# Kernel optimization log

Hardware: AMD Instinct MI355X
Metric: run time of the kernel (lower is better)

The kernel has to match this reference:

```python
import jax, jax.numpy as jnp
import numpy as np
import math

D_MODEL = 32    # channels; expand=1 => d_inner == d_model
D_STATE = 8
D_CONV = 4
DT_RANK = math.ceil(D_MODEL / 16)  # 2


def _layernorm(x, g, b, eps=1e-5):
    m = jnp.mean(x, axis=-1, keepdims=True)
    v = jnp.var(x, axis=-1, keepdims=True)
    return (x - m) * jax.lax.rsqrt(v + eps) * g + b


def _causal_dwconv(x, w, b):
    # x: [B, D, L], w: [D, 1, K] depthwise causal conv (pad K-1 on the left)
    y = jax.lax.conv_general_dilated(
        x, w, window_strides=(1,), padding=[(D_CONV - 1, 0)],
        dimension_numbers=('NCH', 'OIH', 'NCH'),
        feature_group_count=x.shape[1])
    return y + b[None, :, None]


def _ssm_branch(xb, z, conv_w, conv_b, xproj_w, dtproj_w, dtproj_b, A_log, Dp):
    # One mamba_inner (no out_proj) branch. xb, z: [B, D, L]
    Bsz, Dd, L = xb.shape
    u = jax.nn.silu(_causal_dwconv(xb, conv_w, conv_b))              # [B,D,L]
    x_dbl = jnp.einsum('bdl,rd->blr', u, xproj_w)                    # [B,L,R+2N]
    dt = x_dbl[..., :DT_RANK]                                        # [B,L,R]
    Bm = x_dbl[..., DT_RANK:DT_RANK + D_STATE]                       # [B,L,N]
    Cm = x_dbl[..., DT_RANK + D_STATE:]                              # [B,L,N]
    delta = jax.nn.softplus(jnp.einsum('blr,dr->bld', dt, dtproj_w) + dtproj_b)  # [B,L,D]
    A = -jnp.exp(A_log)                                              # [D,N]

    def step(h, inp):
        d_l, u_l, B_l, C_l = inp   # [B,D], [B,D], [B,N], [B,N]
        dA = jnp.exp(d_l[..., None] * A)                             # [B,D,N]
        h = dA * h + (d_l * u_l)[..., None] * B_l[:, None, :]
        y = jnp.einsum('bdn,bn->bd', h, C_l)
        return h, y

    h0 = jnp.zeros((Bsz, Dd, D_STATE), dtype=xb.dtype)
    _, ys = jax.lax.scan(step, h0,
                         (delta.transpose(1, 0, 2), u.transpose(2, 0, 1),
                          Bm.transpose(1, 0, 2), Cm.transpose(1, 0, 2)))
    y = ys.transpose(1, 2, 0)                                        # [B,D,L]
    y = y + Dp[None, :, None] * u
    return y * jax.nn.silu(z)


def _forward(x, w1, b1, ln_g, ln_b, in_proj_w,
             conv_w_f, conv_b_f, xproj_w_f, dtproj_w_f, dtproj_b_f, A_log_f, D_f,
             conv_w_b, conv_b_b, xproj_w_b, dtproj_w_b, dtproj_b_b, A_log_b, D_b,
             norm_g, norm_b, out_proj_w, w2, b2):
    s = jnp.max(x, axis=(2, 3))                                      # AdaptiveMaxPool2d((1,1)) -> [B,L]
    h = s[..., None] * w1[None, None, :, 0] + b1                     # Linear(1, d_model) -> [B,L,D]
    h = _layernorm(h, ln_g, ln_b)
    # Mamba, bimamba v2
    xz = jnp.einsum('bld,ed->bel', h, in_proj_w)                     # [B,2D,L]
    x_f, z_f = jnp.split(xz, 2, axis=1)
    out_f = _ssm_branch(x_f, z_f, conv_w_f, conv_b_f, xproj_w_f,
                        dtproj_w_f, dtproj_b_f, A_log_f, D_f)
    xz_r = jnp.flip(xz, axis=-1)
    x_b, z_b = jnp.split(xz_r, 2, axis=1)
    out_b = _ssm_branch(x_b, z_b, conv_w_b, conv_b_b, xproj_w_b,
                        dtproj_w_b, dtproj_b_b, A_log_b, D_b)
    y = (out_f + jnp.flip(out_b, axis=-1)).transpose(0, 2, 1)        # [B,L,D]
    y = _layernorm(y, norm_g, norm_b) / 2.0                          # use_norm + if_devide_out
    y = jnp.einsum('bld,od->blo', y, out_proj_w)                     # out_proj -> [B,L,D]
    o = jnp.einsum('bld,od->blo', y, w2) + b2                        # Linear(d_model, 1) -> [B,L,1]
    return jax.nn.sigmoid(o)[..., None]                              # [B,L,1,1]


def setup_inputs() -> dict:
    key = jax.random.key(0)
    ks = jax.random.split(key, 16)
    B, Cin, H, W = 16, 128, 256, 256
    D, N, R = D_MODEL, D_STATE, DT_RANK

    def nrm(k, shp, s=0.2):
        return jax.random.normal(k, shp, dtype=jnp.float32) * s

    A_log_init = jnp.log(jnp.arange(1, N + 1, dtype=jnp.float32))[None, :] * jnp.ones((D, 1), jnp.float32)
    return dict(
        x=jax.random.normal(ks[0], (B, Cin, H, W), dtype=jnp.float32),
        w1=nrm(ks[1], (D, 1), 0.5), b1=nrm(ks[2], (D,), 0.1),
        ln_g=jnp.ones((D,), jnp.float32), ln_b=jnp.zeros((D,), jnp.float32),
        in_proj_w=nrm(ks[3], (2 * D, D)),
        conv_w_f=nrm(ks[4], (D, 1, D_CONV)), conv_b_f=nrm(ks[5], (D,), 0.1),
        xproj_w_f=nrm(ks[6], (R + 2 * N, D)),
        dtproj_w_f=nrm(ks[7], (D, R)), dtproj_b_f=nrm(ks[8], (D,), 0.1),
        A_log_f=A_log_init, D_f=jnp.ones((D,), jnp.float32),
        conv_w_b=nrm(ks[9], (D, 1, D_CONV)), conv_b_b=nrm(ks[10], (D,), 0.1),
        xproj_w_b=nrm(ks[11], (R + 2 * N, D)),
        dtproj_w_b=nrm(ks[12], (D, R)), dtproj_b_b=nrm(ks[13], (D,), 0.1),
        A_log_b=A_log_init, D_b=jnp.ones((D,), jnp.float32),
        norm_g=jnp.ones((D,), jnp.float32), norm_b=jnp.zeros((D,), jnp.float32),
        out_proj_w=nrm(ks[14], (D, D)),
        w2=nrm(ks[15], (1, D), 0.5), b2=jnp.zeros((1,), jnp.float32),
    )


def reference(x, w1, b1, ln_g, ln_b, in_proj_w,
              conv_w_f, conv_b_f, xproj_w_f, dtproj_w_f, dtproj_b_f, A_log_f, D_f,
              conv_w_b, conv_b_b, xproj_w_b, dtproj_w_b, dtproj_b_b, A_log_b, D_b,
              norm_g, norm_b, out_proj_w, w2, b2):
    return _forward(x, w1, b1, ln_g, ln_b, in_proj_w,
                    conv_w_f, conv_b_f, xproj_w_f, dtproj_w_f, dtproj_b_f, A_log_f, D_f,
                    conv_w_b, conv_b_b, xproj_w_b, dtproj_w_b, dtproj_b_b, A_log_b, D_b,
                    norm_g, norm_b, out_proj_w, w2, b2)
```

## Files before the change

### kernel.cpp

```cpp
#include <hip/hip_runtime.h>
#include <hip/hip_bf16.h>
#include <math.h>

#define B_SZ 16
#define L_SEQ 128
#define D_M 32
#define HW 65536
#define NROWS (B_SZ * 128)
#define NCHUNK 2

typedef float vfloat4 __attribute__((ext_vector_type(4)));

__device__ float g_part[NROWS * NCHUNK];
__device__ float g_y[2][B_SZ * D_M * L_SEQ];
__device__ int   g_done[B_SZ];

__device__ __forceinline__ float silu_acc(float x) {
    return x / (1.f + __expf(-x));
}
__device__ __forceinline__ float softplusf(float x) {
    return (x > 20.f) ? x : log1pf(__expf(x));
}

__device__ __forceinline__ float row_max(int row) {
    const int r2 = row * NCHUNK;
    return fmaxf(g_part[r2], g_part[r2 + 1]);
}

__device__ __forceinline__ void compute_h(int row, const float* __restrict__ w1,
                                          const float* __restrict__ b1,
                                          const float* __restrict__ lng,
                                          const float* __restrict__ lnb,
                                          float h[D_M]) {
    const float s = row_max(row);
    float mean = 0.f;
#pragma unroll
    for (int d = 0; d < D_M; d++) { h[d] = s * w1[d] + b1[d]; mean += h[d]; }
    mean *= (1.f / D_M);
    float var = 0.f;
#pragma unroll
    for (int d = 0; d < D_M; d++) { float t = h[d] - mean; var += t * t; }
    var *= (1.f / D_M);
    const float rs = rsqrtf(var + 1e-5f);
#pragma unroll
    for (int d = 0; d < D_M; d++) h[d] = (h[d] - mean) * rs * lng[d] + lnb[d];
}

__global__ __launch_bounds__(256) void kmax(const float* __restrict__ x) {
    const int blk = blockIdx.x;
    const vfloat4* __restrict__ p =
        reinterpret_cast<const vfloat4*>(x) + (size_t)blk * 8192;
    const int t = threadIdx.x;
    float m0 = -INFINITY, m1 = -INFINITY, m2 = -INFINITY, m3 = -INFINITY;
#pragma unroll
    for (int i = 0; i < 8192; i += 1024) {
        vfloat4 v0 = __builtin_nontemporal_load(p + i + t);
        vfloat4 v1 = __builtin_nontemporal_load(p + i + t + 256);
        vfloat4 v2 = __builtin_nontemporal_load(p + i + t + 512);
        vfloat4 v3 = __builtin_nontemporal_load(p + i + t + 768);
        m0 = fmaxf(m0, fmaxf(fmaxf(v0.x, v0.y), fmaxf(v0.z, v0.w)));
        m1 = fmaxf(m1, fmaxf(fmaxf(v1.x, v1.y), fmaxf(v1.z, v1.w)));
        m2 = fmaxf(m2, fmaxf(fmaxf(v2.x, v2.y), fmaxf(v2.z, v2.w)));
        m3 = fmaxf(m3, fmaxf(fmaxf(v3.x, v3.y), fmaxf(v3.z, v3.w)));
    }
    float m = fmaxf(fmaxf(m0, m1), fmaxf(m2, m3));
#pragma unroll
    for (int off = 32; off >= 1; off >>= 1)
        m = fmaxf(m, __shfl_xor(m, off));
    __shared__ float sm[4];
    if ((threadIdx.x & 63) == 0) sm[threadIdx.x >> 6] = m;
    __syncthreads();
    if (threadIdx.x == 0)
        g_part[blk] = fmaxf(fmaxf(sm[0], sm[1]), fmaxf(sm[2], sm[3]));
}

__global__ __launch_bounds__(1024) void ktail(
    const float* __restrict__ w1,  const float* __restrict__ b1,
    const float* __restrict__ lng, const float* __restrict__ lnb,
    const float* __restrict__ Win,
    const float* __restrict__ cw_f, const float* __restrict__ cb_f,
    const float* __restrict__ xp_f, const float* __restrict__ dtw_f,
    const float* __restrict__ dtb_f, const float* __restrict__ Al_f,
    const float* __restrict__ Dp_f,
    const float* __restrict__ cw_b, const float* __restrict__ cb_b,
    const float* __restrict__ xp_b, const float* __restrict__ dtw_b,
    const float* __restrict__ dtb_b, const float* __restrict__ Al_b,
    const float* __restrict__ Dp_b,
    const float* __restrict__ ng,  const float* __restrict__ nb,
    const float* __restrict__ Wout, const float* __restrict__ w2,
    const float* __restrict__ b2,  float* __restrict__ out) {
    const int b   = blockIdx.x >> 1;
    const int dir = blockIdx.x & 1;
    const int tid = threadIdx.x;

    const float* cw  = dir ? cw_b  : cw_f;
    const float* cb  = dir ? cb_b  : cb_f;
    const float* xp  = dir ? xp_b  : xp_f;
    const float* dtw = dir ? dtw_b : dtw_f;
    const float* dtb = dir ? dtb_b : dtb_f;
    const float* Al  = dir ? Al_b  : Al_f;
    const float* Dp  = dir ? Dp_b  : Dp_f;

    __shared__ __align__(16) float S[15392];
    __shared__ int s_flag;
    float* sx  = S;
    float* sdl = S;
    float* su  = S + 4352;
    float* sy  = S + 8576;
    float* sdt = S + 12800;
    float* sB  = S + 13056;
    float* sC  = S + 14208;
    float* smm = S + 15360;

    const int l = tid & 127;
    const int q = tid >> 7;
    const int qq = __builtin_amdgcn_readfirstlane(q);

    if (tid < 128) sx[(tid >> 2) * 136 + (tid & 3)] = 0.f;
    if (tid >= 128 && tid < 160) {
        const int d = tid - 128;
        float mm = 0.f;
#pragma unroll
        for (int o = 0; o < D_M; o++) mm += w2[o] * Wout[o * 32 + d];
        smm[d] = mm;
    }
    float h[D_M];
    compute_h(b * L_SEQ + l, w1, b1, lng, lnb, h);

    {
        const int lw = dir ? (127 - l) : l;
#pragma unroll
        for (int k = 0; k < 4; k++) {
            const int e = qq * 4 + k;
            float acc = 0.f;
#pragma unroll
            for (int d = 0; d < D_M; d++) acc += h[d] * Win[e * 32 + d];
            sx[e * 136 + 4 + lw] = acc;
        }
    }

    float zs[4];
#pragma unroll
    for (int k = 0; k < 4; k++) {
        const int d = qq * 4 + k;
        float z = 0.f;
#pragma unroll
        for (int kk = 0; kk < D_M; kk++) z += h[kk] * Win[(32 + d) * 32 + kk];
        zs[k] = silu_acc(z);
    }
    __syncthreads();

    {
        const int d  = tid >> 5;
        const int l0 = (tid & 31) * 4;
        const vfloat4* px = reinterpret_cast<const vfloat4*>(sx + d * 136 + l0);
        vfloat4 a0 = px[0], a1 = px[1];
        float xv[7] = {a0.y, a0.z, a0.w, a1.x, a1.y, a1.z, a1.w};
        const float c0 = cw[d*4+0], c1 = cw[d*4+1], c2 = cw[d*4+2], c3 = cw[d*4+3];
        const float cbd = cb[d];
        float uo[4];
#pragma unroll
        for (int j = 0; j < 4; j++) {
            float acc = cbd + c0*xv[j] + c1*xv[j+1] + c2*xv[j+2] + c3*xv[j+3];
            uo[j] = silu_acc(acc);
        }
        vfloat4 u0 = {uo[0], uo[1], uo[2], uo[3]};
        *reinterpret_cast<vfloat4*>(su + d * 132 + l0) = u0;
    }
    __syncthreads();

    {
        float ul[D_M];
#pragma unroll
        for (int d = 0; d < D_M; d++) ul[d] = su[d * 132 + l];
#pragma unroll
        for (int rep = 0; rep < 3; rep++) {
            const int r = qq + rep * 8;
            if (rep == 2 && qq >= 2) break;
            float acc = 0.f;
#pragma unroll
            for (int d = 0; d < D_M; d++) acc += ul[d] * xp[r * 32 + d];
            if (r < 2)       sdt[l * 2 + r] = acc;
            else if (r < 10) sB[l * 9 + (r - 2)] = acc;
            else             sC[l * 9 + (r - 10)] = acc;
        }
    }
    __syncthreads();

    {
        const float dt0 = sdt[l * 2 + 0], dt1 = sdt[l * 2 + 1];
        const int d0 = qq * 4;
#pragma unroll
        for (int j = 0; j < 4; j++) {
            const int d = d0 + j;
            const float t = dt0 * dtw[d * 2 + 0] + dt1 * dtw[d * 2 + 1] + dtb[d];
            sdl[l * 33 + d] = softplusf(t);
        }
    }
    __syncthreads();

    {
        const int d = tid >> 5;
        const int n = (tid >> 2) & 7;
        const int c = tid & 3;
        const float A  = -__expf(Al[d * 8 + n]);
        const float Dd = Dp[d];
        const int lbase = c * 32;

        float Ac = 1.f, Wc = 0.f;
        for (int i = 0; i < 32; i++) {
            const int ll = lbase + i;
            const float dl = sdl[ll * 33 + d];
            const float ul = su[d * 132 + ll];
            const float w  = (dl * ul) * sB[ll * 9 + n];
            const float dA = __expf(dl * A);
            Wc = dA * Wc + w;
            Ac *= dA;
        }
        float h0 = 0.f;
#pragma unroll
        for (int j = 0; j < 3; j++) {
            const float Aj = __shfl(Ac, j, 4);
            const float Wj = __shfl(Wc, j, 4);
            if (j < c) h0 = Aj * h0 + Wj;
        }
        float hst = h0;
        for (int i = 0; i < 32; i++) {
            const int ll = lbase + i;
            const float dl = sdl[ll * 33 + d];
            const float ul = su[d * 132 + ll];
            const float Bv = sB[ll * 9 + n];
            const float Cv = sC[ll * 9 + n];
            const float dA = __expf(dl * A);
            hst = dA * hst + (dl * ul) * Bv;
            float y = hst * Cv;
            y += __shfl_xor(y, 4);
            y += __shfl_xor(y, 8);
            y += __shfl_xor(y, 16);
            if (n == 0) sy[d * 132 + ll] = y + Dd * ul;
        }
    }
    __syncthreads();

    for (int i = tid; i < 4096; i += 1024) {
        const int d = i >> 7, li = i & 127;
        const int gl = dir ? (127 - li) : li;
        g_y[dir][(b * D_M + d) * L_SEQ + gl] = sy[d * 132 + li];
    }
    __syncthreads();

    if (tid == 0) {
        __threadfence();
        const int old = atomicAdd(&g_done[b], 1);
        const int win = (old == 1);
        if (win) {
            atomicExch(&g_done[b], 0);
            __threadfence();
        }
        s_flag = win;
    }
    __syncthreads();
    if (!s_flag) return;

    {
        float* sv = S;
        const float* y0 = g_y[0] + (size_t)b * D_M * L_SEQ;
        const float* y1 = g_y[1] + (size_t)b * D_M * L_SEQ;

#pragma unroll
        for (int k = 0; k < 4; k++) {
            const int d = qq * 4 + k;
            const float yc = y0[d * L_SEQ + l] + y1[d * L_SEQ + l];
            sv[l * 33 + d] = yc * zs[k];
        }
        __syncthreads();

        if (tid < 128) {
            float vv[D_M];
            float mean = 0.f;
#pragma unroll
            for (int d = 0; d < D_M; d++) { vv[d] = sv[l * 33 + d]; mean += vv[d]; }
            mean *= (1.f / D_M);
            float var = 0.f;
#pragma unroll
            for (int d = 0; d < D_M; d++) { float t = vv[d] - mean; var += t * t; }
            var *= (1.f / D_M);
            const float rs = rsqrtf(var + 1e-5f);

            float acc = b2[0];
#pragma unroll
            for (int d = 0; d < D_M; d++) {
                const float y = ((vv[d] - mean) * rs * ng[d] + nb[d]) * 0.5f;
                acc += y * smm[d];
            }
            out[b * L_SEQ + l] = 1.f / (1.f + __expf(-acc));
        }
    }
}

extern "C" void kernel_launch(void* const* d_in, const int* in_sizes, int n_in,
                              void* d_out, int out_size, void* d_ws, size_t ws_size,
                              hipStream_t stream) {
    const float* x        = (const float*)d_in[0];
    const float* w1       = (const float*)d_in[1];
    const float* b1       = (const float*)d_in[2];
    const float* ln_g     = (const float*)d_in[3];
    const float* ln_b     = (const float*)d_in[4];
    const float* in_proj  = (const float*)d_in[5];
    const float* cw_f     = (const float*)d_in[6];
    const float* cb_f     = (const float*)d_in[7];
    const float* xp_f     = (const float*)d_in[8];
    const float* dtw_f    = (const float*)d_in[9];
    const float* dtb_f    = (const float*)d_in[10];
    const float* Al_f     = (const float*)d_in[11];
    const float* Dp_f     = (const float*)d_in[12];
    const float* cw_b     = (const float*)d_in[13];
    const float* cb_b     = (const float*)d_in[14];
    const float* xp_b     = (const float*)d_in[15];
    const float* dtw_b    = (const float*)d_in[16];
    const float* dtb_b    = (const float*)d_in[17];
    const float* Al_b     = (const float*)d_in[18];
    const float* Dp_b     = (const float*)d_in[19];
    const float* norm_g   = (const float*)d_in[20];
    const float* norm_b   = (const float*)d_in[21];
    const float* Wout     = (const float*)d_in[22];
    const float* w2       = (const float*)d_in[23];
    const float* b2       = (const float*)d_in[24];

    kmax<<<NROWS * NCHUNK, 256, 0, stream>>>(x);
    ktail<<<B_SZ * 2, 1024, 0, stream>>>(w1, b1, ln_g, ln_b, in_proj,
                                         cw_f, cb_f, xp_f, dtw_f, dtb_f, Al_f, Dp_f,
                                         cw_b, cb_b, xp_b, dtw_b, dtb_b, Al_b, Dp_b,
                                         norm_g, norm_b, Wout, w2, b2, (float*)d_out);
}
```

Baseline: 110.9 us.

## Restructure selective scan: per-thread state vector, 8 time chunks, shuffle prefix combine

The scan phase now gives each thread all 8 state entries of one channel over a 16-step chunk, with 8 chunks per channel, instead of one state entry per thread over 32-step chunks. Chunk carries are combined with a log-step shuffle prefix scan, and the C·h reduction becomes an in-register sum rather than cross-lane shuffles. B and C move to a stride-8 layout so they can be read as vectorized LDS loads. Only 256 of the 1024 threads now run the scan, which raises per-thread work and register use and leaves most of the block idle during this phase.

```diff
diff --git a/kernel.cpp b/kernel.cpp
--- a/kernel.cpp
+++ b/kernel.cpp
@@ -101,7 +101,7 @@
     const float* Al  = dir ? Al_b  : Al_f;
     const float* Dp  = dir ? Dp_b  : Dp_f;
 
-    __shared__ __align__(16) float S[15392];
+    __shared__ __align__(16) float S[15136];
     __shared__ int s_flag;
     float* sx  = S;
     float* sdl = S;
@@ -109,8 +109,8 @@
     float* sy  = S + 8576;
     float* sdt = S + 12800;
     float* sB  = S + 13056;
-    float* sC  = S + 14208;
-    float* smm = S + 15360;
+    float* sC  = S + 14080;
+    float* smm = S + 15104;
 
     const int l = tid & 127;
     const int q = tid >> 7;
@@ -181,8 +181,8 @@
 #pragma unroll
             for (int d = 0; d < D_M; d++) acc += ul[d] * xp[r * 32 + d];
             if (r < 2)       sdt[l * 2 + r] = acc;
-            else if (r < 10) sB[l * 9 + (r - 2)] = acc;
-            else             sC[l * 9 + (r - 10)] = acc;
+            else if (r < 10) sB[l * 8 + (r - 2)] = acc;
+            else             sC[l * 8 + (r - 10)] = acc;
         }
     }
     __syncthreads();
@@ -199,45 +199,76 @@
     }
     __syncthreads();
 
-    {
-        const int d = tid >> 5;
-        const int n = (tid >> 2) & 7;
-        const int c = tid & 3;
-        const float A  = -__expf(Al[d * 8 + n]);
+    if (tid < 256) {
+        const int d = tid >> 3;
+        const int c = tid & 7;
+        float An[8];
+        {
+            const vfloat4* ap = reinterpret_cast<const vfloat4*>(Al + d * 8);
+            vfloat4 a0 = ap[0], a1 = ap[1];
+            An[0]=a0.x; An[1]=a0.y; An[2]=a0.z; An[3]=a0.w;
+            An[4]=a1.x; An[5]=a1.y; An[6]=a1.z; An[7]=a1.w;
+#pragma unroll
+            for (int n = 0; n < 8; n++) An[n] = -__expf(An[n]);
+        }
         const float Dd = Dp[d];
-        const int lbase = c * 32;
-
-        float Ac = 1.f, Wc = 0.f;
-        for (int i = 0; i < 32; i++) {
+        const int lbase = c * 16;
+
+        float Ap[8], Wp[8];
+#pragma unroll
+        for (int n = 0; n < 8; n++) { Ap[n] = 1.f; Wp[n] = 0.f; }
+        for (int i = 0; i < 16; i++) {
             const int ll = lbase + i;
             const float dl = sdl[ll * 33 + d];
             const float ul = su[d * 132 + ll];
-            const float w  = (dl * ul) * sB[ll * 9 + n];
-            const float dA = __expf(dl * A);
-            Wc = dA * Wc + w;
-            Ac *= dA;
-        }
-        float h0 = 0.f;
-#pragma unroll
-        for (int j = 0; j < 3; j++) {
-            const float Aj = __shfl(Ac, j, 4);
-            const float Wj = __shfl(Wc, j, 4);
-            if (j < c) h0 = Aj * h0 + Wj;
-        }
-        float hst = h0;
-        for (int i = 0; i < 32; i++) {
+            const float du = dl * ul;
+            const vfloat4* bp = reinterpret_cast<const vfloat4*>(sB + ll * 8);
+            vfloat4 b0 = bp[0], b1 = bp[1];
+            float Bv[8] = {b0.x,b0.y,b0.z,b0.w,b1.x,b1.y,b1.z,b1.w};
+#pragma unroll
+            for (int n = 0; n < 8; n++) {
+                const float dA = __expf(dl * An[n]);
+                Wp[n] = dA * Wp[n] + du * Bv[n];
+                Ap[n] *= dA;
+            }
+        }
+#pragma unroll
+        for (int s = 1; s < 8; s <<= 1) {
+#pragma unroll
+            for (int n = 0; n < 8; n++) {
+                const float Au = __shfl_up(Ap[n], s, 8);
+                const float Wu = __shfl_up(Wp[n], s, 8);
+                if (c >= s) {
+                    Wp[n] = Ap[n] * Wu + Wp[n];
+                    Ap[n] = Ap[n] * Au;
+                }
+            }
+        }
+        float hn[8];
+#pragma unroll
+        for (int n = 0; n < 8; n++) {
+            const float Wu = __shfl_up(Wp[n], 1, 8);
+            hn[n] = (c == 0) ? 0.f : Wu;
+        }
+        for (int i = 0; i < 16; i++) {
             const int ll = lbase + i;
             const float dl = sdl[ll * 33 + d];
             const float ul = su[d * 132 + ll];
-            const float Bv = sB[ll * 9 + n];
-            const float Cv = sC[ll * 9 + n];
-            const float dA = __expf(dl * A);
-            hst = dA * hst + (dl * ul) * Bv;
-            float y = hst * Cv;
-            y += __shfl_xor(y, 4);
-            y += __shfl_xor(y, 8);
-            y += __shfl_xor(y, 16);
-            if (n == 0) sy[d * 132 + ll] = y + Dd * ul;
+            const float du = dl * ul;
+            const vfloat4* bp = reinterpret_cast<const vfloat4*>(sB + ll * 8);
+            const vfloat4* cp = reinterpret_cast<const vfloat4*>(sC + ll * 8);
+            vfloat4 b0 = bp[0], b1 = bp[1];
+            vfloat4 c0 = cp[0], c1 = cp[1];
+            float Bv[8] = {b0.x,b0.y,b0.z,b0.w,b1.x,b1.y,b1.z,b1.w};
+            float Cv[8] = {c0.x,c0.y,c0.z,c0.w,c1.x,c1.y,c1.z,c1.w};
+            float y = 0.f;
+#pragma unroll
+            for (int n = 0; n < 8; n++) {
+                const float dA = __expf(dl * An[n]);
+                hn[n] = dA * hn[n] + du * Bv[n];
+                y += hn[n] * Cv[n];
+            }
+            sy[d * 132 + ll] = y + Dd * ul;
         }
     }
     __syncthreads();
```

Result: faster. 102.4 us (-7.7%).
